# Kernel optimization log

Hardware: AMD Instinct MI355X
Metric: run time of the kernel (lower is better)

The kernel has to match this reference:

```python
import math
import jax, jax.numpy as jnp
import numpy as np

NUM_BUCKETS = 32
MAX_DISTANCE = 128
N_HEADS = 16
D_KV = 64


def _relative_position_bucket(relative_position, num_buckets=NUM_BUCKETS, max_distance=MAX_DISTANCE):
    # bidirectional variant (encoder): half the buckets for each sign
    nb = num_buckets // 2
    n = -relative_position
    ret = (n < 0).astype(jnp.int32) * nb
    n = jnp.abs(n)
    max_exact = nb // 2
    is_small = n < max_exact
    val_if_large = max_exact + (
        jnp.log(jnp.maximum(n, 1).astype(jnp.float32) / max_exact)
        / math.log(max_distance / max_exact)
        * (nb - max_exact)
    ).astype(jnp.int32)
    val_if_large = jnp.minimum(val_if_large, nb - 1)
    return ret + jnp.where(is_small, n, val_if_large)


def setup_inputs() -> dict:
    key = jax.random.key(0)
    ks = jax.random.split(key, 6)
    d_model = 1024
    inner = N_HEADS * D_KV
    scale = 1.0 / math.sqrt(d_model)
    x = jax.random.normal(ks[0], (2, 2048, d_model), dtype=jnp.float32)
    wq = jax.random.normal(ks[1], (d_model, inner), dtype=jnp.float32) * scale
    wk = jax.random.normal(ks[2], (d_model, inner), dtype=jnp.float32) * scale
    wv = jax.random.normal(ks[3], (d_model, inner), dtype=jnp.float32) * scale
    wo = jax.random.normal(ks[4], (inner, d_model), dtype=jnp.float32) * scale
    rel_emb = jax.random.normal(ks[5], (NUM_BUCKETS, N_HEADS), dtype=jnp.float32)
    return {"x": x, "wq": wq, "wk": wk, "wv": wv, "wo": wo, "rel_emb": rel_emb}


def reference(x, wq, wk, wv, wo, rel_emb):
    B, S, D = x.shape
    # QKV projections (no bias, T5 style), split heads -> [B, S, H, Dk]
    q = (x @ wq).reshape(B, S, N_HEADS, D_KV)
    k = (x @ wk).reshape(B, S, N_HEADS, D_KV)
    v = (x @ wv).reshape(B, S, N_HEADS, D_KV)
    # NOTE: T5 does NOT scale by 1/sqrt(d_kv)
    scores = jnp.einsum("bqhd,bkhd->bhqk", q, k)  # [B, H, S, S]
    # relative position bias
    ctx = jnp.arange(S)[:, None]
    mem = jnp.arange(S)[None, :]
    buckets = _relative_position_bucket(mem - ctx)  # [S, S]
    bias = rel_emb[buckets]  # [S, S, H]
    bias = jnp.transpose(bias, (2, 0, 1))[None]  # [1, H, S, S]
    scores = scores + bias
    weights = jax.nn.softmax(scores.astype(jnp.float32), axis=-1).astype(scores.dtype)
    context = jnp.einsum("bhqk,bkhd->bqhd", weights, v).reshape(B, S, N_HEADS * D_KV)
    return context @ wo
```

## Files before the change

### kernel.cpp

```cpp
#include <hip/hip_runtime.h>
#include <hip/hip_bf16.h>

typedef __attribute__((ext_vector_type(8))) _Float16 f16x8;
typedef __attribute__((ext_vector_type(4))) float f32x4;
typedef unsigned short u16;
typedef unsigned int u32;

#define S_LEN 2048
#define NH    16
#define DK    64
#define DMODEL 1024
#define LSTR  40
#define LOG2E 1.44269504f

union F16U { _Float16 h; u16 u; };
__device__ __forceinline__ u16 f2h(float f) {
    F16U v; v.h = (_Float16)f; return v.u;
}

__global__ __launch_bounds__(256) void bias_table_kernel(
    const float* __restrict__ rel_emb, float* __restrict__ tab)
{
    int idx = blockIdx.x * 256 + threadIdx.x;
    int h = idx >> 12;
    int t = idx & 4095;
    int rp = t - 2048;
    int n = -rp;
    int ret = 0;
    if (n < 0) { ret = 16; n = -n; }
    int inner;
    if (n < 8) {
        inner = n;
    } else {
        inner = 8 + (n >= 12) + (n >= 16) + (n >= 23) + (n >= 32)
                  + (n >= 46) + (n >= 64) + (n >= 91);
        if (inner > 15) inner = 15;
    }
    tab[h * 4096 + t] = rel_emb[(ret + inner) * NH + h] * LOG2E;
}

__global__ __launch_bounds__(256) void convert_x(
    const float* __restrict__ X, u16* __restrict__ Xf)
{
    long i8 = ((long)blockIdx.x * 256 + threadIdx.x) * 8;
    float4 a = *(const float4*)&X[i8];
    float4 b = *(const float4*)&X[i8 + 4];
    *(ushort4*)&Xf[i8] =
        make_ushort4(f2h(a.x), f2h(a.y), f2h(a.z), f2h(a.w));
    *(ushort4*)&Xf[i8 + 4] =
        make_ushort4(f2h(b.x), f2h(b.y), f2h(b.z), f2h(b.w));
}

__global__ __launch_bounds__(256) void convert_wT(
    const float* __restrict__ Wq, const float* __restrict__ Wk,
    const float* __restrict__ Wv, const float* __restrict__ Wo,
    u16* __restrict__ WT)
{
    const float* src = (blockIdx.z == 0) ? Wq : (blockIdx.z == 1) ? Wk
                     : (blockIdx.z == 2) ? Wv : Wo;
    u16* dT = WT + (long)blockIdx.z * 1048576;
    __shared__ __align__(16) float T[64 * 68];
    const int k0 = blockIdx.y * 64, n0 = blockIdx.x * 64;
    const int tid = threadIdx.x;
    #pragma unroll
    for (int u = 0; u < 4; u++) {
        int w = tid + u * 256;
        int r = w >> 4, c4 = (w & 15) * 4;
        *(float4*)&T[r * 68 + c4] =
            *(const float4*)&src[(long)(k0 + r) * DMODEL + n0 + c4];
    }
    __syncthreads();
    #pragma unroll
    for (int u = 0; u < 4; u++) {
        int w = tid + u * 256;
        int n = w >> 4, kc = (w & 15) * 4;
        *(ushort4*)&dT[(long)(n0 + n) * DMODEL + k0 + kc] = make_ushort4(
            f2h(T[(kc + 0) * 68 + n]), f2h(T[(kc + 1) * 68 + n]),
            f2h(T[(kc + 2) * 68 + n]), f2h(T[(kc + 3) * 68 + n]));
    }
}

__global__ __launch_bounds__(256, 3) void gemm_qkv_mfma(
    const u16* __restrict__ Xf, const u16* __restrict__ WT,
    u16* __restrict__ Qf, u16* __restrict__ Kf, u16* __restrict__ VT)
{
    const int z = blockIdx.z;
    const u16* BT = WT + (long)z * 1048576;

    __shared__ __align__(16) u16 Ah[128 * LSTR], Bh[128 * LSTR];

    const int tid = threadIdx.x;
    const int wv = tid >> 6, lane = tid & 63;
    const int g = lane >> 4, li = lane & 15;
    const int wr = wv >> 1, wc = wv & 1;
    const int bm = blockIdx.y * 128, bn = blockIdx.x * 128;

    const int srow = tid >> 2, sq8 = (tid & 3) * 8;
    const u16* As0 = &Xf[(long)(bm + srow) * DMODEL + sq8];
    const u16* As1 = &Xf[(long)(bm + srow + 64) * DMODEL + sq8];
    const u16* Bs0 = &BT[(long)(bn + srow) * DMODEL + sq8];
    const u16* Bs1 = &BT[(long)(bn + srow + 64) * DMODEL + sq8];
    u16* AL0 = &Ah[srow * LSTR + sq8];
    u16* AL1 = &Ah[(srow + 64) * LSTR + sq8];
    u16* BL0 = &Bh[srow * LSTR + sq8];
    u16* BL1 = &Bh[(srow + 64) * LSTR + sq8];

    f32x4 acc[4][4];
    #pragma unroll
    for (int i = 0; i < 4; i++)
        #pragma unroll
        for (int j = 0; j < 4; j++) acc[i][j] = (f32x4){0.f, 0.f, 0.f, 0.f};

    *(uint4*)AL0 = *(const uint4*)As0;
    *(uint4*)AL1 = *(const uint4*)As1;
    *(uint4*)BL0 = *(const uint4*)Bs0;
    *(uint4*)BL1 = *(const uint4*)Bs1;
    __syncthreads();

    for (int k0 = 0; k0 < DMODEL; k0 += 32) {
        const bool have = (k0 + 32) < DMODEL;
        uint4 na0, na1, nb0, nb1;
        if (have) {
            na0 = *(const uint4*)(As0 + k0 + 32);
            na1 = *(const uint4*)(As1 + k0 + 32);
            nb0 = *(const uint4*)(Bs0 + k0 + 32);
            nb1 = *(const uint4*)(Bs1 + k0 + 32);
        }

        f16x8 a_h[4], b_h[4];
        #pragma unroll
        for (int i = 0; i < 4; i++)
            a_h[i] = *(const f16x8*)&Ah[(wr * 64 + i * 16 + li) * LSTR + g * 8];
        #pragma unroll
        for (int j = 0; j < 4; j++)
            b_h[j] = *(const f16x8*)&Bh[(wc * 64 + j * 16 + li) * LSTR + g * 8];
        #pragma unroll
        for (int i = 0; i < 4; i++)
            #pragma unroll
            for (int j = 0; j < 4; j++)
                acc[i][j] = __builtin_amdgcn_mfma_f32_16x16x32_f16(
                    a_h[i], b_h[j], acc[i][j], 0, 0, 0);

        if (have) {
            __syncthreads();
            *(uint4*)AL0 = na0; *(uint4*)AL1 = na1;
            *(uint4*)BL0 = nb0; *(uint4*)BL1 = nb1;
            __syncthreads();
        }
    }

    if (z == 2) {
        #pragma unroll
        for (int i = 0; i < 4; i++) {
            int s_base = bm + wr * 64 + i * 16 + g * 4;
            int bb = s_base >> 11, s = s_base & 2047;
            #pragma unroll
            for (int j = 0; j < 4; j++) {
                int gcol = bn + wc * 64 + j * 16 + li;
                int hh = gcol >> 6, d = gcol & 63;
                long idx = (((long)(bb * NH + hh)) * DK + d) * S_LEN + s;
                *(ushort4*)&VT[idx] = make_ushort4(
                    f2h(acc[i][j][0]), f2h(acc[i][j][1]),
                    f2h(acc[i][j][2]), f2h(acc[i][j][3]));
            }
        }
    } else {
        u16* O = (z == 0) ? Qf : Kf;
        #pragma unroll
        for (int i = 0; i < 4; i++) {
            #pragma unroll
            for (int r = 0; r < 4; r++) {
                int grow = bm + wr * 64 + i * 16 + g * 4 + r;
                int bb = grow >> 11, s = grow & 2047;
                #pragma unroll
                for (int j = 0; j < 4; j++) {
                    int gcol = bn + wc * 64 + j * 16 + li;
                    int hh = gcol >> 6, d = gcol & 63;
                    long idx = (((long)(bb * NH + hh)) * S_LEN + s) * DK + d;
                    O[idx] = f2h(acc[i][j][r]);
                }
            }
        }
    }
}

__global__ __launch_bounds__(256, 3) void gemm_out_mfma(
    const u16* __restrict__ Ab, const u16* __restrict__ WT,
    float* __restrict__ O)
{
    const u16* BT = WT + 3L * 1048576;
    __shared__ __align__(16) u16 Ah[128 * LSTR], Bh[128 * LSTR];

    const int tid = threadIdx.x;
    const int wv = tid >> 6, lane = tid & 63;
    const int g = lane >> 4, li = lane & 15;
    const int wr = wv >> 1, wc = wv & 1;
    const int bm = blockIdx.y * 128, bn = blockIdx.x * 128;

    const int srow = tid >> 2, sq8 = (tid & 3) * 8;
    const u16* As0 = &Ab[(long)(bm + srow) * DMODEL + sq8];
    const u16* As1 = &Ab[(long)(bm + srow + 64) * DMODEL + sq8];
    const u16* Bs0 = &BT[(long)(bn + srow) * DMODEL + sq8];
    const u16* Bs1 = &BT[(long)(bn + srow + 64) * DMODEL + sq8];
    u16* AL0 = &Ah[srow * LSTR + sq8];
    u16* AL1 = &Ah[(srow + 64) * LSTR + sq8];
    u16* BL0 = &Bh[srow * LSTR + sq8];
    u16* BL1 = &Bh[(srow + 64) * LSTR + sq8];

    f32x4 acc[4][4];
    #pragma unroll
    for (int i = 0; i < 4; i++)
        #pragma unroll
        for (int j = 0; j < 4; j++) acc[i][j] = (f32x4){0.f, 0.f, 0.f, 0.f};

    *(uint4*)AL0 = *(const uint4*)As0;
    *(uint4*)AL1 = *(const uint4*)As1;
    *(uint4*)BL0 = *(const uint4*)Bs0;
    *(uint4*)BL1 = *(const uint4*)Bs1;
    __syncthreads();

    for (int k0 = 0; k0 < DMODEL; k0 += 32) {
        const bool have = (k0 + 32) < DMODEL;
        uint4 na0, na1, nb0, nb1;
        if (have) {
            na0 = *(const uint4*)(As0 + k0 + 32);
            na1 = *(const uint4*)(As1 + k0 + 32);
            nb0 = *(const uint4*)(Bs0 + k0 + 32);
            nb1 = *(const uint4*)(Bs1 + k0 + 32);
        }

        f16x8 a_h[4], b_h[4];
        #pragma unroll
        for (int i = 0; i < 4; i++)
            a_h[i] = *(const f16x8*)&Ah[(wr * 64 + i * 16 + li) * LSTR + g * 8];
        #pragma unroll
        for (int j = 0; j < 4; j++)
            b_h[j] = *(const f16x8*)&Bh[(wc * 64 + j * 16 + li) * LSTR + g * 8];
        #pragma unroll
        for (int i = 0; i < 4; i++)
            #pragma unroll
            for (int j = 0; j < 4; j++)
                acc[i][j] = __builtin_amdgcn_mfma_f32_16x16x32_f16(
                    a_h[i], b_h[j], acc[i][j], 0, 0, 0);

        if (have) {
            __syncthreads();
            *(uint4*)AL0 = na0; *(uint4*)AL1 = na1;
            *(uint4*)BL0 = nb0; *(uint4*)BL1 = nb1;
            __syncthreads();
        }
    }

    #pragma unroll
    for (int i = 0; i < 4; i++)
        #pragma unroll
        for (int r = 0; r < 4; r++) {
            int grow = bm + wr * 64 + i * 16 + g * 4 + r;
            #pragma unroll
            for (int j = 0; j < 4; j++) {
                int gcol = bn + wc * 64 + j * 16 + li;
                O[(long)grow * DMODEL + gcol] = acc[i][j][r];
            }
        }
}

#define APAD 72

__global__ __launch_bounds__(256, 4) void attn_mfma(
    const u16* __restrict__ Qf, const u16* __restrict__ Kf,
    const u16* __restrict__ VT, const float* __restrict__ tab,
    u16* __restrict__ ctxb)
{
    __shared__ __align__(16) u16 Ks[64 * APAD];
    __shared__ __align__(16) u16 Vs[64 * APAD];
    __shared__ __align__(16) u16 Ps[64 * APAD];
    __shared__ float biasS[128];

    const int tid = threadIdx.x;
    const int wv = tid >> 6, lane = tid & 63;
    const int g = lane >> 4, li = lane & 15;
    const int qblk = blockIdx.x & 31;
    const int h = (blockIdx.x >> 5) & 15;
    const int b = blockIdx.x >> 9;
    const int q0 = qblk * 64;
    const long bh = b * NH + h;
    const int qloc = wv * 16 + li;

    const u16* KhG = Kf + bh * (S_LEN * DK);
    const u16* VtG = VT + bh * (DK * S_LEN);
    const float* th = tab + h * 4096;

    const int srow = tid >> 3, sc8 = (tid & 7) * 8;

    f16x8 q0f, q1f;
    {
        long qrow = bh * S_LEN + q0 + qloc;
        const u16* ph = Qf + qrow * DK + g * 8;
        q0f = *(const f16x8*)ph;  q1f = *(const f16x8*)(ph + 32);
    }

    *(uint4*)&Ks[srow * APAD + sc8] =
        *(const uint4*)&KhG[(long)srow * DK + sc8];
    *(uint4*)&Ks[(srow + 32) * APAD + sc8] =
        *(const uint4*)&KhG[(long)(srow + 32) * DK + sc8];
    *(uint4*)&Vs[srow * APAD + sc8] =
        *(const uint4*)&VtG[(long)srow * S_LEN + sc8];
    *(uint4*)&Vs[(srow + 32) * APAD + sc8] =
        *(const uint4*)&VtG[(long)(srow + 32) * S_LEN + sc8];
    if (tid < 128) {
        int idx = tid - 63 - q0 + 2048;
        idx = idx < 0 ? 0 : (idx > 4095 ? 4095 : idx);
        biasS[tid] = th[idx];
    }
    __syncthreads();

    f32x4 Oc[4];
    #pragma unroll
    for (int n = 0; n < 4; n++) Oc[n] = (f32x4){0.f, 0.f, 0.f, 0.f};
    float mP = -1e30f, lR = 0.f;

    for (int kt0 = 0; kt0 < S_LEN; kt0 += 64) {
        const int ktn = kt0 + 64;
        const bool havenext = ktn < S_LEN;

        uint4 nk0, nk1, nv0, nv1; float nb = 0.f;
        if (havenext) {
            nk0 = *(const uint4*)&KhG[(long)(ktn + srow) * DK + sc8];
            nk1 = *(const uint4*)&KhG[(long)(ktn + srow + 32) * DK + sc8];
            nv0 = *(const uint4*)&VtG[(long)srow * S_LEN + ktn + sc8];
            nv1 = *(const uint4*)&VtG[(long)(srow + 32) * S_LEN + ktn + sc8];
            if (tid < 128) {
                int idx = ktn + tid - 63 - q0 + 2048;
                idx = idx < 0 ? 0 : (idx > 4095 ? 4095 : idx);
                nb = th[idx];
            }
        }

        f32x4 Sa[4];
        __builtin_amdgcn_s_setprio(1);
        #pragma unroll
        for (int m = 0; m < 4; m++) {
            const u16* kp = &Ks[(m * 16 + li) * APAD + g * 8];
            f16x8 k0 = *(const f16x8*)kp, k1 = *(const f16x8*)(kp + 32);
            f32x4 s = (f32x4){0.f, 0.f, 0.f, 0.f};
            s = __builtin_amdgcn_mfma_f32_16x16x32_f16(k0, q0f, s, 0, 0, 0);
            s = __builtin_amdgcn_mfma_f32_16x16x32_f16(k1, q1f, s, 0, 0, 0);
            Sa[m] = s;
        }
        __builtin_amdgcn_s_setprio(0);

        #pragma unroll
        for (int m = 0; m < 4; m++)
            #pragma unroll
            for (int r = 0; r < 4; r++)
                Sa[m][r] = fmaf(Sa[m][r], LOG2E,
                                biasS[m * 16 + g * 4 + r + 63 - qloc]);

        float mm[4];
        #pragma unroll
        for (int m = 0; m < 4; m++)
            mm[m] = fmaxf(fmaxf(Sa[m][0], Sa[m][1]),
                          fmaxf(Sa[m][2], Sa[m][3]));
        float pm = fmaxf(fmaxf(mm[0], mm[1]), fmaxf(mm[2], mm[3]));
        pm = fmaxf(pm, __shfl_xor(pm, 16));
        pm = fmaxf(pm, __shfl_xor(pm, 32));

        if (__any(pm > mP)) {
            float mn = fmaxf(mP, pm);
            float alpha = __builtin_amdgcn_exp2f(mP - mn);
            mP = mn;
            lR *= alpha;
            float aO[4];
            #pragma unroll
            for (int r = 0; r < 4; r++) aO[r] = __shfl(alpha, g * 4 + r);
            #pragma unroll
            for (int n = 0; n < 4; n++)
                #pragma unroll
                for (int r = 0; r < 4; r++) Oc[n][r] *= aO[r];
        }

        float sm[4];
        #pragma unroll
        for (int m = 0; m < 4; m++) {
            #pragma unroll
            for (int r = 0; r < 4; r++)
                Sa[m][r] = __builtin_amdgcn_exp2f(Sa[m][r] - mP);
            sm[m] = (Sa[m][0] + Sa[m][1]) + (Sa[m][2] + Sa[m][3]);
        }
        float ls = (sm[0] + sm[1]) + (sm[2] + sm[3]);
        ls += __shfl_xor(ls, 16);
        ls += __shfl_xor(ls, 32);
        lR += ls;

        #pragma unroll
        for (int m = 0; m < 4; m++)
            *(ushort4*)&Ps[qloc * APAD + m * 16 + g * 4] = make_ushort4(
                f2h(Sa[m][0]), f2h(Sa[m][1]), f2h(Sa[m][2]), f2h(Sa[m][3]));

        {
            const u16* pp = &Ps[qloc * APAD + g * 8];
            f16x8 p0 = *(const f16x8*)pp, p1 = *(const f16x8*)(pp + 32);
            __builtin_amdgcn_s_setprio(1);
            #pragma unroll
            for (int n = 0; n < 4; n++) {
                const u16* vp = &Vs[(n * 16 + li) * APAD + g * 8];
                f16x8 v0 = *(const f16x8*)vp, v1 = *(const f16x8*)(vp + 32);
                Oc[n] = __builtin_amdgcn_mfma_f32_16x16x32_f16(p0, v0, Oc[n], 0, 0, 0);
                Oc[n] = __builtin_amdgcn_mfma_f32_16x16x32_f16(p1, v1, Oc[n], 0, 0, 0);
            }
            __builtin_amdgcn_s_setprio(0);
        }

        if (havenext) {
            __syncthreads();
            *(uint4*)&Ks[srow * APAD + sc8] = nk0;
            *(uint4*)&Ks[(srow + 32) * APAD + sc8] = nk1;
            *(uint4*)&Vs[srow * APAD + sc8] = nv0;
            *(uint4*)&Vs[(srow + 32) * APAD + sc8] = nv1;
            if (tid < 128) biasS[tid] = nb;
            __syncthreads();
        }
    }

    float linv = 1.0f / lR;
    float iv[4];
    #pragma unroll
    for (int r = 0; r < 4; r++) iv[r] = __shfl(linv, g * 4 + r);
    #pragma unroll
    for (int n = 0; n < 4; n++)
        #pragma unroll
        for (int r = 0; r < 4; r++)
            ctxb[((long)(b * S_LEN + q0 + wv * 16 + g * 4 + r)) * DMODEL
                 + h * DK + n * 16 + li] = f2h(Oc[n][r] * iv[r]);
}

extern "C" void kernel_launch(void* const* d_in, const int* in_sizes, int n_in,
                              void* d_out, int out_size, void* d_ws, size_t ws_size,
                              hipStream_t stream)
{
    const float* x    = (const float*)d_in[0];
    const float* wq   = (const float*)d_in[1];
    const float* wk   = (const float*)d_in[2];
    const float* wv   = (const float*)d_in[3];
    const float* wo   = (const float*)d_in[4];
    const float* rel  = (const float*)d_in[5];

    u16* W0 = (u16*)d_ws;
    u16* Xf  = W0;
    u16* Qf  = W0 + 4194304;
    u16* Kf  = W0 + 8388608;
    u16* VT  = W0 + 12582912;
    u16* WT  = W0 + 16777216;
    float* tab = (float*)(W0 + 20971520);
    u16* ctxb = Xf;

    bias_table_kernel<<<dim3(256), dim3(256), 0, stream>>>(rel, tab);
    convert_x<<<dim3(2048), dim3(256), 0, stream>>>(x, Xf);
    convert_wT<<<dim3(16, 16, 4), dim3(256), 0, stream>>>(wq, wk, wv, wo, WT);
    gemm_qkv_mfma<<<dim3(8, 32, 3), dim3(256), 0, stream>>>(Xf, WT, Qf, Kf, VT);
    attn_mfma<<<dim3(1024), dim3(256), 0, stream>>>(Qf, Kf, VT, tab, ctxb);
    gemm_out_mfma<<<dim3(8, 32), dim3(256), 0, stream>>>(ctxb, WT, (float*)d_out);
}
```

Baseline: 223.5 us.

## Double-buffer LDS tiles in GEMMs and attention, load V directly from global

Both GEMM kernels now use double-buffered shared memory tiles. The next tile is written to the alternate buffer while the current one is consumed, which cuts two barriers per k-step down to one. The attention kernel double-buffers K and the bias slice in LDS, and loads V fragments straight from global memory into registers instead of staging them through LDS. It also remaps block indices so consecutive blocks spread across heads and batches. The change costs more LDS per block and adds register pressure from the prefetched V fragments, and the global V loads may expose latency.

```diff
diff --git a/kernel.cpp b/kernel.cpp
--- a/kernel.cpp
+++ b/kernel.cpp
@@ -12,6 +12,7 @@
 #define DMODEL 1024
 #define LSTR  40
 #define LOG2E 1.44269504f
+#define NTILES (S_LEN / 64)
 
 union F16U { _Float16 h; u16 u; };
 __device__ __forceinline__ u16 f2h(float f) {
@@ -87,7 +88,7 @@
     const int z = blockIdx.z;
     const u16* BT = WT + (long)z * 1048576;
 
-    __shared__ __align__(16) u16 Ah[128 * LSTR], Bh[128 * LSTR];
+    __shared__ __align__(16) u16 Ah[2][128 * LSTR], Bh[2][128 * LSTR];
 
     const int tid = threadIdx.x;
     const int wv = tid >> 6, lane = tid & 63;
@@ -97,13 +98,10 @@
 
     const int srow = tid >> 2, sq8 = (tid & 3) * 8;
     const u16* As0 = &Xf[(long)(bm + srow) * DMODEL + sq8];
-    const u16* As1 = &Xf[(long)(bm + srow + 64) * DMODEL + sq8];
+    const u16* As1 = As0 + 64 * DMODEL;
     const u16* Bs0 = &BT[(long)(bn + srow) * DMODEL + sq8];
-    const u16* Bs1 = &BT[(long)(bn + srow + 64) * DMODEL + sq8];
-    u16* AL0 = &Ah[srow * LSTR + sq8];
-    u16* AL1 = &Ah[(srow + 64) * LSTR + sq8];
-    u16* BL0 = &Bh[srow * LSTR + sq8];
-    u16* BL1 = &Bh[(srow + 64) * LSTR + sq8];
+    const u16* Bs1 = Bs0 + 64 * DMODEL;
+    const int l0 = srow * LSTR + sq8, l1 = (srow + 64) * LSTR + sq8;
 
     f32x4 acc[4][4];
     #pragma unroll
@@ -111,29 +109,39 @@
         #pragma unroll
         for (int j = 0; j < 4; j++) acc[i][j] = (f32x4){0.f, 0.f, 0.f, 0.f};
 
-    *(uint4*)AL0 = *(const uint4*)As0;
-    *(uint4*)AL1 = *(const uint4*)As1;
-    *(uint4*)BL0 = *(const uint4*)Bs0;
-    *(uint4*)BL1 = *(const uint4*)Bs1;
+    *(uint4*)&Ah[0][l0] = *(const uint4*)As0;
+    *(uint4*)&Ah[0][l1] = *(const uint4*)As1;
+    *(uint4*)&Bh[0][l0] = *(const uint4*)Bs0;
+    *(uint4*)&Bh[0][l1] = *(const uint4*)Bs1;
+    uint4 na0 = *(const uint4*)(As0 + 32);
+    uint4 na1 = *(const uint4*)(As1 + 32);
+    uint4 nb0 = *(const uint4*)(Bs0 + 32);
+    uint4 nb1 = *(const uint4*)(Bs1 + 32);
     __syncthreads();
 
+    int cur = 0;
     for (int k0 = 0; k0 < DMODEL; k0 += 32) {
-        const bool have = (k0 + 32) < DMODEL;
-        uint4 na0, na1, nb0, nb1;
-        if (have) {
-            na0 = *(const uint4*)(As0 + k0 + 32);
-            na1 = *(const uint4*)(As1 + k0 + 32);
-            nb0 = *(const uint4*)(Bs0 + k0 + 32);
-            nb1 = *(const uint4*)(Bs1 + k0 + 32);
-        }
-
         f16x8 a_h[4], b_h[4];
         #pragma unroll
         for (int i = 0; i < 4; i++)
-            a_h[i] = *(const f16x8*)&Ah[(wr * 64 + i * 16 + li) * LSTR + g * 8];
+            a_h[i] = *(const f16x8*)&Ah[cur][(wr * 64 + i * 16 + li) * LSTR + g * 8];
         #pragma unroll
         for (int j = 0; j < 4; j++)
-            b_h[j] = *(const f16x8*)&Bh[(wc * 64 + j * 16 + li) * LSTR + g * 8];
+            b_h[j] = *(const f16x8*)&Bh[cur][(wc * 64 + j * 16 + li) * LSTR + g * 8];
+
+        if (k0 + 32 < DMODEL) {
+            *(uint4*)&Ah[cur ^ 1][l0] = na0;
+            *(uint4*)&Ah[cur ^ 1][l1] = na1;
+            *(uint4*)&Bh[cur ^ 1][l0] = nb0;
+            *(uint4*)&Bh[cur ^ 1][l1] = nb1;
+        }
+        if (k0 + 64 < DMODEL) {
+            na0 = *(const uint4*)(As0 + k0 + 64);
+            na1 = *(const uint4*)(As1 + k0 + 64);
+            nb0 = *(const uint4*)(Bs0 + k0 + 64);
+            nb1 = *(const uint4*)(Bs1 + k0 + 64);
+        }
+
         #pragma unroll
         for (int i = 0; i < 4; i++)
             #pragma unroll
@@ -141,12 +149,8 @@
                 acc[i][j] = __builtin_amdgcn_mfma_f32_16x16x32_f16(
                     a_h[i], b_h[j], acc[i][j], 0, 0, 0);
 
-        if (have) {
-            __syncthreads();
-            *(uint4*)AL0 = na0; *(uint4*)AL1 = na1;
-            *(uint4*)BL0 = nb0; *(uint4*)BL1 = nb1;
-            __syncthreads();
-        }
+        __syncthreads();
+        cur ^= 1;
     }
 
     if (z == 2) {
@@ -189,7 +193,7 @@
     float* __restrict__ O)
 {
     const u16* BT = WT + 3L * 1048576;
-    __shared__ __align__(16) u16 Ah[128 * LSTR], Bh[128 * LSTR];
+    __shared__ __align__(16) u16 Ah[2][128 * LSTR], Bh[2][128 * LSTR];
 
     const int tid = threadIdx.x;
     const int wv = tid >> 6, lane = tid & 63;
@@ -199,13 +203,10 @@
 
     const int srow = tid >> 2, sq8 = (tid & 3) * 8;
     const u16* As0 = &Ab[(long)(bm + srow) * DMODEL + sq8];
-    const u16* As1 = &Ab[(long)(bm + srow + 64) * DMODEL + sq8];
+    const u16* As1 = As0 + 64 * DMODEL;
     const u16* Bs0 = &BT[(long)(bn + srow) * DMODEL + sq8];
-    const u16* Bs1 = &BT[(long)(bn + srow + 64) * DMODEL + sq8];
-    u16* AL0 = &Ah[srow * LSTR + sq8];
-    u16* AL1 = &Ah[(srow + 64) * LSTR + sq8];
-    u16* BL0 = &Bh[srow * LSTR + sq8];
-    u16* BL1 = &Bh[(srow + 64) * LSTR + sq8];
+    const u16* Bs1 = Bs0 + 64 * DMODEL;
+    const int l0 = srow * LSTR + sq8, l1 = (srow + 64) * LSTR + sq8;
 
     f32x4 acc[4][4];
     #pragma unroll
@@ -213,29 +214,39 @@
         #pragma unroll
         for (int j = 0; j < 4; j++) acc[i][j] = (f32x4){0.f, 0.f, 0.f, 0.f};
 
-    *(uint4*)AL0 = *(const uint4*)As0;
-    *(uint4*)AL1 = *(const uint4*)As1;
-    *(uint4*)BL0 = *(const uint4*)Bs0;
-    *(uint4*)BL1 = *(const uint4*)Bs1;
+    *(uint4*)&Ah[0][l0] = *(const uint4*)As0;
+    *(uint4*)&Ah[0][l1] = *(const uint4*)As1;
+    *(uint4*)&Bh[0][l0] = *(const uint4*)Bs0;
+    *(uint4*)&Bh[0][l1] = *(const uint4*)Bs1;
+    uint4 na0 = *(const uint4*)(As0 + 32);
+    uint4 na1 = *(const uint4*)(As1 + 32);
+    uint4 nb0 = *(const uint4*)(Bs0 + 32);
+    uint4 nb1 = *(const uint4*)(Bs1 + 32);
     __syncthreads();
 
+    int cur = 0;
     for (int k0 = 0; k0 < DMODEL; k0 += 32) {
-        const bool have = (k0 + 32) < DMODEL;
-        uint4 na0, na1, nb0, nb1;
-        if (have) {
-            na0 = *(const uint4*)(As0 + k0 + 32);
-            na1 = *(const uint4*)(As1 + k0 + 32);
-            nb0 = *(const uint4*)(Bs0 + k0 + 32);
-            nb1 = *(const uint4*)(Bs1 + k0 + 32);
-        }
-
         f16x8 a_h[4], b_h[4];
         #pragma unroll
         for (int i = 0; i < 4; i++)
-            a_h[i] = *(const f16x8*)&Ah[(wr * 64 + i * 16 + li) * LSTR + g * 8];
+            a_h[i] = *(const f16x8*)&Ah[cur][(wr * 64 + i * 16 + li) * LSTR + g * 8];
         #pragma unroll
         for (int j = 0; j < 4; j++)
-            b_h[j] = *(const f16x8*)&Bh[(wc * 64 + j * 16 + li) * LSTR + g * 8];
+            b_h[j] = *(const f16x8*)&Bh[cur][(wc * 64 + j * 16 + li) * LSTR + g * 8];
+
+        if (k0 + 32 < DMODEL) {
+            *(uint4*)&Ah[cur ^ 1][l0] = na0;
+            *(uint4*)&Ah[cur ^ 1][l1] = na1;
+            *(uint4*)&Bh[cur ^ 1][l0] = nb0;
+            *(uint4*)&Bh[cur ^ 1][l1] = nb1;
+        }
+        if (k0 + 64 < DMODEL) {
+            na0 = *(const uint4*)(As0 + k0 + 64);
+            na1 = *(const uint4*)(As1 + k0 + 64);
+            nb0 = *(const uint4*)(Bs0 + k0 + 64);
+            nb1 = *(const uint4*)(Bs1 + k0 + 64);
+        }
+
         #pragma unroll
         for (int i = 0; i < 4; i++)
             #pragma unroll
@@ -243,12 +254,8 @@
                 acc[i][j] = __builtin_amdgcn_mfma_f32_16x16x32_f16(
                     a_h[i], b_h[j], acc[i][j], 0, 0, 0);
 
-        if (have) {
-            __syncthreads();
-            *(uint4*)AL0 = na0; *(uint4*)AL1 = na1;
-            *(uint4*)BL0 = nb0; *(uint4*)BL1 = nb1;
-            __syncthreads();
-        }
+        __syncthreads();
+        cur ^= 1;
     }
 
     #pragma unroll
@@ -271,17 +278,18 @@
     const u16* __restrict__ VT, const float* __restrict__ tab,
     u16* __restrict__ ctxb)
 {
-    __shared__ __align__(16) u16 Ks[64 * APAD];
-    __shared__ __align__(16) u16 Vs[64 * APAD];
+    __shared__ __align__(16) u16 Ks[2][64 * APAD];
     __shared__ __align__(16) u16 Ps[64 * APAD];
-    __shared__ float biasS[128];
+    __shared__ float biasS[2][128];
 
     const int tid = threadIdx.x;
     const int wv = tid >> 6, lane = tid & 63;
     const int g = lane >> 4, li = lane & 15;
-    const int qblk = blockIdx.x & 31;
-    const int h = (blockIdx.x >> 5) & 15;
-    const int b = blockIdx.x >> 9;
+
+    const int nbid = (blockIdx.x & 7) * 128 + (blockIdx.x >> 3);
+    const int qblk = nbid & 31;
+    const int h = (nbid >> 5) & 15;
+    const int b = nbid >> 9;
     const int q0 = qblk * 64;
     const long bh = b * NH + h;
     const int qloc = wv * 16 + li;
@@ -291,6 +299,8 @@
     const float* th = tab + h * 4096;
 
     const int srow = tid >> 3, sc8 = (tid & 7) * 8;
+    const u16* Kst = KhG + (long)srow * DK + sc8;
+    const u16* vpb = VtG + (long)li * S_LEN + g * 8;
 
     f16x8 q0f, q1f;
     {
@@ -299,18 +309,20 @@
         q0f = *(const f16x8*)ph;  q1f = *(const f16x8*)(ph + 32);
     }
 
-    *(uint4*)&Ks[srow * APAD + sc8] =
-        *(const uint4*)&KhG[(long)srow * DK + sc8];
-    *(uint4*)&Ks[(srow + 32) * APAD + sc8] =
-        *(const uint4*)&KhG[(long)(srow + 32) * DK + sc8];
-    *(uint4*)&Vs[srow * APAD + sc8] =
-        *(const uint4*)&VtG[(long)srow * S_LEN + sc8];
-    *(uint4*)&Vs[(srow + 32) * APAD + sc8] =
-        *(const uint4*)&VtG[(long)(srow + 32) * S_LEN + sc8];
+    *(uint4*)&Ks[0][srow * APAD + sc8] = *(const uint4*)Kst;
+    *(uint4*)&Ks[0][(srow + 32) * APAD + sc8] = *(const uint4*)(Kst + 32 * DK);
     if (tid < 128) {
         int idx = tid - 63 - q0 + 2048;
         idx = idx < 0 ? 0 : (idx > 4095 ? 4095 : idx);
-        biasS[tid] = th[idx];
+        biasS[0][tid] = th[idx];
+    }
+    uint4 nk0 = *(const uint4*)(Kst + 64 * DK);
+    uint4 nk1 = *(const uint4*)(Kst + 96 * DK);
+    float nb = 0.f;
+    if (tid < 128) {
+        int idx = 64 + tid - 63 - q0 + 2048;
+        idx = idx < 0 ? 0 : (idx > 4095 ? 4095 : idx);
+        nb = th[idx];
     }
     __syncthreads();
 
@@ -319,28 +331,23 @@
     for (int n = 0; n < 4; n++) Oc[n] = (f32x4){0.f, 0.f, 0.f, 0.f};
     float mP = -1e30f, lR = 0.f;
 
-    for (int kt0 = 0; kt0 < S_LEN; kt0 += 64) {
-        const int ktn = kt0 + 64;
-        const bool havenext = ktn < S_LEN;
-
-        uint4 nk0, nk1, nv0, nv1; float nb = 0.f;
-        if (havenext) {
-            nk0 = *(const uint4*)&KhG[(long)(ktn + srow) * DK + sc8];
-            nk1 = *(const uint4*)&KhG[(long)(ktn + srow + 32) * DK + sc8];
-            nv0 = *(const uint4*)&VtG[(long)srow * S_LEN + ktn + sc8];
-            nv1 = *(const uint4*)&VtG[(long)(srow + 32) * S_LEN + ktn + sc8];
-            if (tid < 128) {
-                int idx = ktn + tid - 63 - q0 + 2048;
-                idx = idx < 0 ? 0 : (idx > 4095 ? 4095 : idx);
-                nb = th[idx];
-            }
+    int cur = 0;
+    for (int t = 0; t < NTILES; ++t) {
+        const int kt0 = t * 64;
+
+        f16x8 va[4], vb[4];
+        #pragma unroll
+        for (int n = 0; n < 4; n++) {
+            const u16* vp = vpb + (long)n * (16 * S_LEN) + kt0;
+            va[n] = *(const f16x8*)vp;
+            vb[n] = *(const f16x8*)(vp + 32);
         }
 
         f32x4 Sa[4];
         __builtin_amdgcn_s_setprio(1);
         #pragma unroll
         for (int m = 0; m < 4; m++) {
-            const u16* kp = &Ks[(m * 16 + li) * APAD + g * 8];
+            const u16* kp = &Ks[cur][(m * 16 + li) * APAD + g * 8];
             f16x8 k0 = *(const f16x8*)kp, k1 = *(const f16x8*)(kp + 32);
             f32x4 s = (f32x4){0.f, 0.f, 0.f, 0.f};
             s = __builtin_amdgcn_mfma_f32_16x16x32_f16(k0, q0f, s, 0, 0, 0);
@@ -349,12 +356,28 @@
         }
         __builtin_amdgcn_s_setprio(0);
 
+        if (t + 1 < NTILES) {
+            *(uint4*)&Ks[cur ^ 1][srow * APAD + sc8] = nk0;
+            *(uint4*)&Ks[cur ^ 1][(srow + 32) * APAD + sc8] = nk1;
+            if (tid < 128) biasS[cur ^ 1][tid] = nb;
+        }
+        if (t + 2 < NTILES) {
+            const u16* kp2 = Kst + (long)(kt0 + 128) * DK;
+            nk0 = *(const uint4*)kp2;
+            nk1 = *(const uint4*)(kp2 + 32 * DK);
+            if (tid < 128) {
+                int idx = kt0 + 128 + tid - 63 - q0 + 2048;
+                idx = idx < 0 ? 0 : (idx > 4095 ? 4095 : idx);
+                nb = th[idx];
+            }
+        }
+
         #pragma unroll
         for (int m = 0; m < 4; m++)
             #pragma unroll
             for (int r = 0; r < 4; r++)
                 Sa[m][r] = fmaf(Sa[m][r], LOG2E,
-                                biasS[m * 16 + g * 4 + r + 63 - qloc]);
+                                biasS[cur][m * 16 + g * 4 + r + 63 - qloc]);
 
         float mm[4];
         #pragma unroll
@@ -403,23 +426,14 @@
             __builtin_amdgcn_s_setprio(1);
             #pragma unroll
             for (int n = 0; n < 4; n++) {
-                const u16* vp = &Vs[(n * 16 + li) * APAD + g * 8];
-                f16x8 v0 = *(const f16x8*)vp, v1 = *(const f16x8*)(vp + 32);
-                Oc[n] = __builtin_amdgcn_mfma_f32_16x16x32_f16(p0, v0, Oc[n], 0, 0, 0);
-                Oc[n] = __builtin_amdgcn_mfma_f32_16x16x32_f16(p1, v1, Oc[n], 0, 0, 0);
+                Oc[n] = __builtin_amdgcn_mfma_f32_16x16x32_f16(p0, va[n], Oc[n], 0, 0, 0);
+                Oc[n] = __builtin_amdgcn_mfma_f32_16x16x32_f16(p1, vb[n], Oc[n], 0, 0, 0);
             }
             __builtin_amdgcn_s_setprio(0);
         }
 
-        if (havenext) {
-            __syncthreads();
-            *(uint4*)&Ks[srow * APAD + sc8] = nk0;
-            *(uint4*)&Ks[(srow + 32) * APAD + sc8] = nk1;
-            *(uint4*)&Vs[srow * APAD + sc8] = nv0;
-            *(uint4*)&Vs[(srow + 32) * APAD + sc8] = nv1;
-            if (tid < 128) biasS[tid] = nb;
-            __syncthreads();
-        }
+        __syncthreads();
+        cur ^= 1;
     }
 
     float linv = 1.0f / lR;
```

Measured after the change: 276.1 us. +23.5%, slower.

## Double-buffer K/V in attention, shuffle P in registers, read bias directly

Applied to the files above, without the earlier changes.

The attention kernel now double-buffers the K and V shared-memory tiles and prefetches two tiles ahead. This replaces the two barriers per iteration with one. The P matrix is moved from accumulator layout into operand layout with cross-lane shuffles instead of a round trip through shared memory, and the bias values are read directly from the global table per thread rather than staged in shared memory. Block indices are also remapped to spread heads and batches across XCDs. The cost is more registers, which may reduce occupancy, and scattered global bias loads.

```diff
diff --git a/kernel.cpp b/kernel.cpp
--- a/kernel.cpp
+++ b/kernel.cpp
@@ -12,6 +12,7 @@
 #define DMODEL 1024
 #define LSTR  40
 #define LOG2E 1.44269504f
+#define NTILES (S_LEN / 64)
 
 union F16U { _Float16 h; u16 u; };
 __device__ __forceinline__ u16 f2h(float f) {
@@ -97,9 +98,9 @@
 
     const int srow = tid >> 2, sq8 = (tid & 3) * 8;
     const u16* As0 = &Xf[(long)(bm + srow) * DMODEL + sq8];
-    const u16* As1 = &Xf[(long)(bm + srow + 64) * DMODEL + sq8];
+    const u16* As1 = As0 + 64 * DMODEL;
     const u16* Bs0 = &BT[(long)(bn + srow) * DMODEL + sq8];
-    const u16* Bs1 = &BT[(long)(bn + srow + 64) * DMODEL + sq8];
+    const u16* Bs1 = Bs0 + 64 * DMODEL;
     u16* AL0 = &Ah[srow * LSTR + sq8];
     u16* AL1 = &Ah[(srow + 64) * LSTR + sq8];
     u16* BL0 = &Bh[srow * LSTR + sq8];
@@ -199,9 +200,9 @@
 
     const int srow = tid >> 2, sq8 = (tid & 3) * 8;
     const u16* As0 = &Ab[(long)(bm + srow) * DMODEL + sq8];
-    const u16* As1 = &Ab[(long)(bm + srow + 64) * DMODEL + sq8];
+    const u16* As1 = As0 + 64 * DMODEL;
     const u16* Bs0 = &BT[(long)(bn + srow) * DMODEL + sq8];
-    const u16* Bs1 = &BT[(long)(bn + srow + 64) * DMODEL + sq8];
+    const u16* Bs1 = Bs0 + 64 * DMODEL;
     u16* AL0 = &Ah[srow * LSTR + sq8];
     u16* AL1 = &Ah[(srow + 64) * LSTR + sq8];
     u16* BL0 = &Bh[srow * LSTR + sq8];
@@ -271,26 +272,29 @@
     const u16* __restrict__ VT, const float* __restrict__ tab,
     u16* __restrict__ ctxb)
 {
-    __shared__ __align__(16) u16 Ks[64 * APAD];
-    __shared__ __align__(16) u16 Vs[64 * APAD];
-    __shared__ __align__(16) u16 Ps[64 * APAD];
-    __shared__ float biasS[128];
+    __shared__ __align__(16) u16 Ks[2][64 * APAD];
+    __shared__ __align__(16) u16 Vs[2][64 * APAD];
 
     const int tid = threadIdx.x;
     const int wv = tid >> 6, lane = tid & 63;
     const int g = lane >> 4, li = lane & 15;
-    const int qblk = blockIdx.x & 31;
-    const int h = (blockIdx.x >> 5) & 15;
-    const int b = blockIdx.x >> 9;
+
+    const int nbid = (blockIdx.x & 7) * 128 + (blockIdx.x >> 3);
+    const int qblk = nbid & 31;
+    const int h = (nbid >> 5) & 15;
+    const int b = nbid >> 9;
     const int q0 = qblk * 64;
     const long bh = b * NH + h;
     const int qloc = wv * 16 + li;
 
     const u16* KhG = Kf + bh * (S_LEN * DK);
     const u16* VtG = VT + bh * (DK * S_LEN);
-    const float* th = tab + h * 4096;
+    const float* thq = tab + h * 4096 + 2048 - q0 - qloc + g * 4;
 
     const int srow = tid >> 3, sc8 = (tid & 7) * 8;
+    const u16* Kst = KhG + (long)srow * DK + sc8;
+    const u16* Vst0 = VtG + (long)srow * S_LEN + sc8;
+    const u16* Vst1 = VtG + (long)(srow + 32) * S_LEN + sc8;
 
     f16x8 q0f, q1f;
     {
@@ -299,19 +303,14 @@
         q0f = *(const f16x8*)ph;  q1f = *(const f16x8*)(ph + 32);
     }
 
-    *(uint4*)&Ks[srow * APAD + sc8] =
-        *(const uint4*)&KhG[(long)srow * DK + sc8];
-    *(uint4*)&Ks[(srow + 32) * APAD + sc8] =
-        *(const uint4*)&KhG[(long)(srow + 32) * DK + sc8];
-    *(uint4*)&Vs[srow * APAD + sc8] =
-        *(const uint4*)&VtG[(long)srow * S_LEN + sc8];
-    *(uint4*)&Vs[(srow + 32) * APAD + sc8] =
-        *(const uint4*)&VtG[(long)(srow + 32) * S_LEN + sc8];
-    if (tid < 128) {
-        int idx = tid - 63 - q0 + 2048;
-        idx = idx < 0 ? 0 : (idx > 4095 ? 4095 : idx);
-        biasS[tid] = th[idx];
-    }
+    *(uint4*)&Ks[0][srow * APAD + sc8] = *(const uint4*)Kst;
+    *(uint4*)&Ks[0][(srow + 32) * APAD + sc8] = *(const uint4*)(Kst + 32 * DK);
+    *(uint4*)&Vs[0][srow * APAD + sc8] = *(const uint4*)Vst0;
+    *(uint4*)&Vs[0][(srow + 32) * APAD + sc8] = *(const uint4*)Vst1;
+    uint4 nk0 = *(const uint4*)(Kst + 64 * DK);
+    uint4 nk1 = *(const uint4*)(Kst + 96 * DK);
+    uint4 nv0 = *(const uint4*)(Vst0 + 64);
+    uint4 nv1 = *(const uint4*)(Vst1 + 64);
     __syncthreads();
 
     f32x4 Oc[4];
@@ -319,28 +318,23 @@
     for (int n = 0; n < 4; n++) Oc[n] = (f32x4){0.f, 0.f, 0.f, 0.f};
     float mP = -1e30f, lR = 0.f;
 
-    for (int kt0 = 0; kt0 < S_LEN; kt0 += 64) {
-        const int ktn = kt0 + 64;
-        const bool havenext = ktn < S_LEN;
-
-        uint4 nk0, nk1, nv0, nv1; float nb = 0.f;
-        if (havenext) {
-            nk0 = *(const uint4*)&KhG[(long)(ktn + srow) * DK + sc8];
-            nk1 = *(const uint4*)&KhG[(long)(ktn + srow + 32) * DK + sc8];
-            nv0 = *(const uint4*)&VtG[(long)srow * S_LEN + ktn + sc8];
-            nv1 = *(const uint4*)&VtG[(long)(srow + 32) * S_LEN + ktn + sc8];
-            if (tid < 128) {
-                int idx = ktn + tid - 63 - q0 + 2048;
-                idx = idx < 0 ? 0 : (idx > 4095 ? 4095 : idx);
-                nb = th[idx];
-            }
-        }
+    int cur = 0;
+    for (int t = 0; t < NTILES; ++t) {
+        const int kt0 = t * 64;
+
+        const float* tb = thq + kt0;
+        float bia[4][4];
+        #pragma unroll
+        for (int m = 0; m < 4; m++)
+            #pragma unroll
+            for (int r = 0; r < 4; r++)
+                bia[m][r] = tb[m * 16 + r];
 
         f32x4 Sa[4];
         __builtin_amdgcn_s_setprio(1);
         #pragma unroll
         for (int m = 0; m < 4; m++) {
-            const u16* kp = &Ks[(m * 16 + li) * APAD + g * 8];
+            const u16* kp = &Ks[cur][(m * 16 + li) * APAD + g * 8];
             f16x8 k0 = *(const f16x8*)kp, k1 = *(const f16x8*)(kp + 32);
             f32x4 s = (f32x4){0.f, 0.f, 0.f, 0.f};
             s = __builtin_amdgcn_mfma_f32_16x16x32_f16(k0, q0f, s, 0, 0, 0);
@@ -349,12 +343,25 @@
         }
         __builtin_amdgcn_s_setprio(0);
 
+        if (t + 1 < NTILES) {
+            *(uint4*)&Ks[cur ^ 1][srow * APAD + sc8] = nk0;
+            *(uint4*)&Ks[cur ^ 1][(srow + 32) * APAD + sc8] = nk1;
+            *(uint4*)&Vs[cur ^ 1][srow * APAD + sc8] = nv0;
+            *(uint4*)&Vs[cur ^ 1][(srow + 32) * APAD + sc8] = nv1;
+        }
+        if (t + 2 < NTILES) {
+            const u16* kp2 = Kst + (long)(kt0 + 128) * DK;
+            nk0 = *(const uint4*)kp2;
+            nk1 = *(const uint4*)(kp2 + 32 * DK);
+            nv0 = *(const uint4*)(Vst0 + kt0 + 128);
+            nv1 = *(const uint4*)(Vst1 + kt0 + 128);
+        }
+
         #pragma unroll
         for (int m = 0; m < 4; m++)
             #pragma unroll
             for (int r = 0; r < 4; r++)
-                Sa[m][r] = fmaf(Sa[m][r], LOG2E,
-                                biasS[m * 16 + g * 4 + r + 63 - qloc]);
+                Sa[m][r] = fmaf(Sa[m][r], LOG2E, bia[m][r]);
 
         float mm[4];
         #pragma unroll
@@ -392,34 +399,57 @@
         ls += __shfl_xor(ls, 32);
         lR += ls;
 
-        #pragma unroll
-        for (int m = 0; m < 4; m++)
-            *(ushort4*)&Ps[qloc * APAD + m * 16 + g * 4] = make_ushort4(
-                f2h(Sa[m][0]), f2h(Sa[m][1]), f2h(Sa[m][2]), f2h(Sa[m][3]));
-
+        u32 y0, y1, y2, y3, y4, y5, y6, y7;
         {
-            const u16* pp = &Ps[qloc * APAD + g * 8];
-            f16x8 p0 = *(const f16x8*)pp, p1 = *(const f16x8*)(pp + 32);
-            __builtin_amdgcn_s_setprio(1);
-            #pragma unroll
-            for (int n = 0; n < 4; n++) {
-                const u16* vp = &Vs[(n * 16 + li) * APAD + g * 8];
-                f16x8 v0 = *(const f16x8*)vp, v1 = *(const f16x8*)(vp + 32);
-                Oc[n] = __builtin_amdgcn_mfma_f32_16x16x32_f16(p0, v0, Oc[n], 0, 0, 0);
-                Oc[n] = __builtin_amdgcn_mfma_f32_16x16x32_f16(p1, v1, Oc[n], 0, 0, 0);
-            }
-            __builtin_amdgcn_s_setprio(0);
-        }
-
-        if (havenext) {
-            __syncthreads();
-            *(uint4*)&Ks[srow * APAD + sc8] = nk0;
-            *(uint4*)&Ks[(srow + 32) * APAD + sc8] = nk1;
-            *(uint4*)&Vs[srow * APAD + sc8] = nv0;
-            *(uint4*)&Vs[(srow + 32) * APAD + sc8] = nv1;
-            if (tid < 128) biasS[tid] = nb;
-            __syncthreads();
-        }
+            u32 p00 = f2h(Sa[0][0]) | ((u32)f2h(Sa[0][1]) << 16);
+            u32 p01 = f2h(Sa[0][2]) | ((u32)f2h(Sa[0][3]) << 16);
+            u32 p10 = f2h(Sa[1][0]) | ((u32)f2h(Sa[1][1]) << 16);
+            u32 p11 = f2h(Sa[1][2]) | ((u32)f2h(Sa[1][3]) << 16);
+            u32 p20 = f2h(Sa[2][0]) | ((u32)f2h(Sa[2][1]) << 16);
+            u32 p21 = f2h(Sa[2][2]) | ((u32)f2h(Sa[2][3]) << 16);
+            u32 p30 = f2h(Sa[3][0]) | ((u32)f2h(Sa[3][1]) << 16);
+            u32 p31 = f2h(Sa[3][2]) | ((u32)f2h(Sa[3][3]) << 16);
+            y0 = p00; y1 = p01; y2 = p10; y3 = p11;
+            y4 = p20; y5 = p21; y6 = p30; y7 = p31;
+        }
+        {
+            bool hi = (lane & 32) != 0;
+            u32 s0 = hi ? y0 : y2, s1 = hi ? y1 : y3;
+            u32 s4 = hi ? y4 : y6, s5 = hi ? y5 : y7;
+            u32 r0 = __shfl_xor((int)s0, 32);
+            u32 r1 = __shfl_xor((int)s1, 32);
+            u32 r4 = __shfl_xor((int)s4, 32);
+            u32 r5 = __shfl_xor((int)s5, 32);
+            if (hi) { y0 = r0; y1 = r1; y4 = r4; y5 = r5; }
+            else    { y2 = r0; y3 = r1; y6 = r4; y7 = r5; }
+        }
+        {
+            bool hi = (lane & 16) != 0;
+            u32 s0 = hi ? y0 : y2, s1 = hi ? y1 : y3;
+            u32 s4 = hi ? y4 : y6, s5 = hi ? y5 : y7;
+            u32 r0 = __shfl_xor((int)s0, 16);
+            u32 r1 = __shfl_xor((int)s1, 16);
+            u32 r4 = __shfl_xor((int)s4, 16);
+            u32 r5 = __shfl_xor((int)s5, 16);
+            if (hi) { y0 = r0; y1 = r1; y4 = r4; y5 = r5; }
+            else    { y2 = r0; y3 = r1; y6 = r4; y7 = r5; }
+        }
+        union { uint4 u; f16x8 h; } P0, P1;
+        P0.u = make_uint4(y0, y1, y2, y3);
+        P1.u = make_uint4(y4, y5, y6, y7);
+
+        __builtin_amdgcn_s_setprio(1);
+        #pragma unroll
+        for (int n = 0; n < 4; n++) {
+            const u16* vp = &Vs[cur][(n * 16 + li) * APAD + g * 8];
+            f16x8 v0 = *(const f16x8*)vp, v1 = *(const f16x8*)(vp + 32);
+            Oc[n] = __builtin_amdgcn_mfma_f32_16x16x32_f16(P0.h, v0, Oc[n], 0, 0, 0);
+            Oc[n] = __builtin_amdgcn_mfma_f32_16x16x32_f16(P1.h, v1, Oc[n], 0, 0, 0);
+        }
+        __builtin_amdgcn_s_setprio(0);
+
+        __syncthreads();
+        cur ^= 1;
     }
 
     float linv = 1.0f / lR;
```

New measurement: 217.3 us. 1.03x faster.
